# Kernel optimization log

Measured on AMD Instinct MI355X. Metric: run time of the kernel, lower is better.

## Reference

```python
import jax, jax.numpy as jnp
import numpy as np

FEATURES = 1024
DEPTH = int(np.floor(np.log2(FEATURES)))  # 10
NODES = 2 ** DEPTH - 1                    # 1023


def _unit_rows(key, shape):
    w = jax.random.normal(key, shape, dtype=jnp.float32)
    return w / jnp.linalg.norm(w, axis=-1, keepdims=True)


def setup_inputs() -> dict:
    key = jax.random.key(0)
    k_x, k_X, k_Y = jax.random.split(key, 3)
    oldx = jax.random.normal(k_x, (8, 4096, FEATURES), dtype=jnp.float32)
    X = _unit_rows(k_X, (NODES, FEATURES))  # hyperspherical-shell init
    Y = _unit_rows(k_Y, (NODES, FEATURES))
    return {"oldx": oldx, "X": X, "Y": Y}


def reference(oldx, X, Y):
    features = X.shape[-1]
    x = oldx.reshape(-1, features)            # [B, F]
    B = x.shape[0]
    cur = jnp.zeros((B,), dtype=jnp.int32)    # per-sample tree node
    y = jnp.zeros_like(x)
    for _ in range(DEPTH):                    # fixed small depth loop (10)
        Xc = X[cur]                           # [B, F] data-dependent gather
        lam = jnp.einsum('bi,bi->b', x, Xc)   # [B]
        y = y + lam[:, None] * Y[cur]         # [B, F]
        cur = cur * 2 + 1 + (lam > 0).astype(jnp.int32)
    return y.reshape(oldx.shape)
```

## Files before the change

kernel.cpp:

```cpp
#include <hip/hip_runtime.h>

#define FEAT 1024
#define DEPTH 10
#define NLEAF 1024
#define NODES (NLEAF - 1)

typedef float f32x4 __attribute__((ext_vector_type(4)));

__global__ __launch_bounds__(256) void path_kernel(
    const float* __restrict__ x,
    const float* __restrict__ Xw,
    float* __restrict__ lam_out,
    int* __restrict__ leaf_out,
    int* __restrict__ counts,
    int nsamples)
{
    const int wave = threadIdx.x >> 6;
    const int lane = threadIdx.x & 63;
    const int s = blockIdx.x * 4 + wave;
    if (s >= nsamples) return;

    const float* xp = x + (size_t)s * FEAT;
    f32x4 xv[4];
#pragma unroll
    for (int k = 0; k < 4; ++k)
        xv[k] = __builtin_nontemporal_load(
            reinterpret_cast<const f32x4*>(xp + (lane + 64 * k) * 4));

    int cur = 0;
#pragma unroll
    for (int d = 0; d < DEPTH; ++d) {
        const float* Xr = Xw + (size_t)cur * FEAT;
        double p0 = 0.0, p1 = 0.0, p2 = 0.0, p3 = 0.0;
#pragma unroll
        for (int k = 0; k < 4; ++k) {
            f32x4 xc = *reinterpret_cast<const f32x4*>(Xr + (lane + 64 * k) * 4);
            p0 += (double)xv[k][0] * (double)xc[0];
            p1 += (double)xv[k][1] * (double)xc[1];
            p2 += (double)xv[k][2] * (double)xc[2];
            p3 += (double)xv[k][3] * (double)xc[3];
        }
        double p = (p0 + p1) + (p2 + p3);
#pragma unroll
        for (int off = 32; off >= 1; off >>= 1)
            p += __shfl_xor(p, off, 64);

        if (lane == 0) lam_out[(size_t)s * DEPTH + d] = (float)p;
        cur = 2 * cur + 1 + (p > 0.0 ? 1 : 0);
    }

    if (lane == 0) {
        leaf_out[s] = cur;
        atomicAdd(&counts[cur - NODES], 1);
    }
}

__global__ __launch_bounds__(1024) void scan_kernel(
    const int* __restrict__ counts, int* __restrict__ offs, int* __restrict__ cursor)
{
    __shared__ int a[NLEAF], b[NLEAF];
    const int t = threadIdx.x;
    a[t] = counts[t];
    __syncthreads();
    int* src = a; int* dst = b;
#pragma unroll
    for (int off = 1; off < NLEAF; off <<= 1) {
        dst[t] = (t >= off) ? (src[t] + src[t - off]) : src[t];
        __syncthreads();
        int* tmp = src; src = dst; dst = tmp;
    }
    const int excl = (t == 0) ? 0 : src[t - 1];
    offs[t] = excl;
    cursor[t] = excl;
}

__global__ __launch_bounds__(256) void scatter_kernel(
    const int* __restrict__ leaf, int* __restrict__ cursor,
    int* __restrict__ order, int nsamples)
{
    int i = blockIdx.x * 256 + threadIdx.x;
    if (i < nsamples) {
        const int b = leaf[i] - NODES;
        const int pos = atomicAdd(&cursor[b], 1);
        order[pos] = i;
    }
}

__global__ __launch_bounds__(256) void emit_kernel(
    const float* __restrict__ Yw,
    const float* __restrict__ lam,
    const int* __restrict__ order,
    const int* __restrict__ offs,
    const int* __restrict__ counts,
    float* __restrict__ out)
{
    __shared__ float ylds[DEPTH][FEAT];
    const int b = blockIdx.x;
    const int leafPlus = b + NLEAF;

#pragma unroll
    for (int d = 0; d < DEPTH; ++d) {
        const int node = (leafPlus >> (DEPTH - d)) - 1;
        reinterpret_cast<f32x4*>(ylds[d])[threadIdx.x] =
            reinterpret_cast<const f32x4*>(Yw + (size_t)node * FEAT)[threadIdx.x];
    }
    __syncthreads();

    const int start = offs[b];
    const int cnt = counts[b];
    const int wave = threadIdx.x >> 6;
    const int lane = threadIdx.x & 63;

    for (int i = wave; i < cnt; i += 4) {
        const int s = order[start + i];
        float lm[DEPTH];
#pragma unroll
        for (int d = 0; d < DEPTH; ++d)
            lm[d] = lam[(size_t)s * DEPTH + d];

        float* op = out + (size_t)s * FEAT;
#pragma unroll
        for (int k = 0; k < 4; ++k) {
            f32x4 o = (f32x4)(0.f);
#pragma unroll
            for (int d = 0; d < DEPTH; ++d)
                o += lm[d] * reinterpret_cast<const f32x4*>(ylds[d])[lane + 64 * k];
            __builtin_nontemporal_store(o, reinterpret_cast<f32x4*>(op + 4 * (lane + 64 * k)));
        }
    }
}

__global__ __launch_bounds__(256) void fff_fallback(
    const float* __restrict__ x, const float* __restrict__ Xw,
    const float* __restrict__ Yw, float* __restrict__ out, int nsamples)
{
    const int wave = threadIdx.x >> 6, lane = threadIdx.x & 63;
    const int s = blockIdx.x * 4 + wave;
    if (s >= nsamples) return;
    const float* xp = x + (size_t)s * FEAT;
    f32x4 xv[4], acc[4];
#pragma unroll
    for (int k = 0; k < 4; ++k) {
        xv[k] = *reinterpret_cast<const f32x4*>(xp + (lane + 64 * k) * 4);
        acc[k] = (f32x4)(0.f);
    }
    int cur = 0;
#pragma unroll
    for (int d = 0; d < DEPTH; ++d) {
        const float* Xr = Xw + (size_t)cur * FEAT;
        double p = 0.0;
#pragma unroll
        for (int k = 0; k < 4; ++k) {
            f32x4 xc = *reinterpret_cast<const f32x4*>(Xr + (lane + 64 * k) * 4);
            p += (double)xv[k][0] * (double)xc[0];
            p += (double)xv[k][1] * (double)xc[1];
            p += (double)xv[k][2] * (double)xc[2];
            p += (double)xv[k][3] * (double)xc[3];
        }
#pragma unroll
        for (int off = 32; off >= 1; off >>= 1) p += __shfl_xor(p, off, 64);
        const float lamv = (float)p;
        const float* Yr = Yw + (size_t)cur * FEAT;
#pragma unroll
        for (int k = 0; k < 4; ++k) {
            f32x4 yc = *reinterpret_cast<const f32x4*>(Yr + (lane + 64 * k) * 4);
            acc[k] += lamv * yc;
        }
        cur = 2 * cur + 1 + (p > 0.0 ? 1 : 0);
    }
    float* op = out + (size_t)s * FEAT;
#pragma unroll
    for (int k = 0; k < 4; ++k)
        *reinterpret_cast<f32x4*>(op + 4 * (lane + 64 * k)) = acc[k];
}

extern "C" void kernel_launch(void* const* d_in, const int* in_sizes, int n_in,
                              void* d_out, int out_size, void* d_ws, size_t ws_size,
                              hipStream_t stream) {
    const float* oldx = (const float*)d_in[0];
    const float* Xw   = (const float*)d_in[1];
    const float* Yw   = (const float*)d_in[2];
    float* out = (float*)d_out;

    const int ns = in_sizes[0] / FEAT;

    const size_t lamB  = (size_t)ns * DEPTH * sizeof(float);
    const size_t leafB = (size_t)ns * sizeof(int);
    const size_t cntB  = NLEAF * sizeof(int);
    const size_t need  = lamB + leafB + 3 * cntB + leafB;

    if (ws_size < need) {
        fff_fallback<<<(ns + 3) / 4, 256, 0, stream>>>(oldx, Xw, Yw, out, ns);
        return;
    }

    char* w = (char*)d_ws;
    float* lam    = (float*)w;  w += lamB;
    int*   leaf   = (int*)w;    w += leafB;
    int*   counts = (int*)w;    w += cntB;
    int*   offs   = (int*)w;    w += cntB;
    int*   cursor = (int*)w;    w += cntB;
    int*   order  = (int*)w;

    hipMemsetAsync(counts, 0, cntB, stream);
    path_kernel<<<(ns + 3) / 4, 256, 0, stream>>>(oldx, Xw, lam, leaf, counts, ns);
    scan_kernel<<<1, 1024, 0, stream>>>(counts, offs, cursor);
    scatter_kernel<<<(ns + 255) / 256, 256, 0, stream>>>(leaf, cursor, order, ns);
    emit_kernel<<<NLEAF, 256, 0, stream>>>(Yw, lam, order, offs, counts, out);
}
```

Baseline: 122.7 us.

## Stage shallow tree rows in LDS, widen blocks, shuffle-broadcast lambdas in emit

The path kernel now runs 1024-thread blocks covering 16 samples each, and copies the first 15 tree rows of X (levels 0-3) into 60KB of shared memory. The first four depth steps read from LDS and the deeper ones still read global memory. The emit kernel moves to 512 threads and 8 waves, spreads the Y-row staging over a strided loop, and loads the ten lambdas with one lane-parallel load followed by shuffles. The aim is to cut redundant global and L2 reads of hot shallow rows and scalar lambda loads. In exchange every block must first stage 60KB, and the large LDS footprint limits occupancy.

New measurement: 126.5 us. +3.1%, slower.

```diff
diff --git a/kernel.cpp b/kernel.cpp
--- a/kernel.cpp
+++ b/kernel.cpp
@@ -4,10 +4,11 @@
 #define DEPTH 10
 #define NLEAF 1024
 #define NODES (NLEAF - 1)
+#define SHALLOW_ROWS 15
 
 typedef float f32x4 __attribute__((ext_vector_type(4)));
 
-__global__ __launch_bounds__(256) void path_kernel(
+__global__ __launch_bounds__(1024) void path_kernel(
     const float* __restrict__ x,
     const float* __restrict__ Xw,
     float* __restrict__ lam_out,
@@ -15,9 +16,16 @@
     int* __restrict__ counts,
     int nsamples)
 {
-    const int wave = threadIdx.x >> 6;
-    const int lane = threadIdx.x & 63;
-    const int s = blockIdx.x * 4 + wave;
+    __shared__ float xlds[SHALLOW_ROWS * FEAT];
+
+    const int tid = threadIdx.x;
+    for (int i = tid; i < SHALLOW_ROWS * (FEAT / 4); i += 1024)
+        reinterpret_cast<f32x4*>(xlds)[i] = reinterpret_cast<const f32x4*>(Xw)[i];
+    __syncthreads();
+
+    const int wave = tid >> 6;
+    const int lane = tid & 63;
+    const int s = blockIdx.x * 16 + wave;
     if (s >= nsamples) return;
 
     const float* xp = x + (size_t)s * FEAT;
@@ -28,9 +36,10 @@
             reinterpret_cast<const f32x4*>(xp + (lane + 64 * k) * 4));
 
     int cur = 0;
-#pragma unroll
-    for (int d = 0; d < DEPTH; ++d) {
-        const float* Xr = Xw + (size_t)cur * FEAT;
+
+#pragma unroll
+    for (int d = 0; d < 4; ++d) {
+        const float* Xr = xlds + (size_t)cur * FEAT;
         double p0 = 0.0, p1 = 0.0, p2 = 0.0, p3 = 0.0;
 #pragma unroll
         for (int k = 0; k < 4; ++k) {
@@ -44,7 +53,26 @@
 #pragma unroll
         for (int off = 32; off >= 1; off >>= 1)
             p += __shfl_xor(p, off, 64);
-
+        if (lane == 0) lam_out[(size_t)s * DEPTH + d] = (float)p;
+        cur = 2 * cur + 1 + (p > 0.0 ? 1 : 0);
+    }
+
+#pragma unroll
+    for (int d = 4; d < DEPTH; ++d) {
+        const float* Xr = Xw + (size_t)cur * FEAT;
+        double p0 = 0.0, p1 = 0.0, p2 = 0.0, p3 = 0.0;
+#pragma unroll
+        for (int k = 0; k < 4; ++k) {
+            f32x4 xc = *reinterpret_cast<const f32x4*>(Xr + (lane + 64 * k) * 4);
+            p0 += (double)xv[k][0] * (double)xc[0];
+            p1 += (double)xv[k][1] * (double)xc[1];
+            p2 += (double)xv[k][2] * (double)xc[2];
+            p3 += (double)xv[k][3] * (double)xc[3];
+        }
+        double p = (p0 + p1) + (p2 + p3);
+#pragma unroll
+        for (int off = 32; off >= 1; off >>= 1)
+            p += __shfl_xor(p, off, 64);
         if (lane == 0) lam_out[(size_t)s * DEPTH + d] = (float)p;
         cur = 2 * cur + 1 + (p > 0.0 ? 1 : 0);
     }
@@ -86,7 +114,7 @@
     }
 }
 
-__global__ __launch_bounds__(256) void emit_kernel(
+__global__ __launch_bounds__(512) void emit_kernel(
     const float* __restrict__ Yw,
     const float* __restrict__ lam,
     const int* __restrict__ order,
@@ -98,11 +126,12 @@
     const int b = blockIdx.x;
     const int leafPlus = b + NLEAF;
 
-#pragma unroll
-    for (int d = 0; d < DEPTH; ++d) {
+    for (int i = threadIdx.x; i < DEPTH * (FEAT / 4); i += 512) {
+        const int d = i >> 8;
+        const int c = i & 255;
         const int node = (leafPlus >> (DEPTH - d)) - 1;
-        reinterpret_cast<f32x4*>(ylds[d])[threadIdx.x] =
-            reinterpret_cast<const f32x4*>(Yw + (size_t)node * FEAT)[threadIdx.x];
+        reinterpret_cast<f32x4*>(ylds[d])[c] =
+            reinterpret_cast<const f32x4*>(Yw + (size_t)node * FEAT)[c];
     }
     __syncthreads();
 
@@ -111,12 +140,14 @@
     const int wave = threadIdx.x >> 6;
     const int lane = threadIdx.x & 63;
 
-    for (int i = wave; i < cnt; i += 4) {
+    for (int i = wave; i < cnt; i += 8) {
         const int s = order[start + i];
+
+        float lv = (lane < DEPTH) ? lam[(size_t)s * DEPTH + lane] : 0.0f;
         float lm[DEPTH];
 #pragma unroll
         for (int d = 0; d < DEPTH; ++d)
-            lm[d] = lam[(size_t)s * DEPTH + d];
+            lm[d] = __shfl(lv, d, 64);
 
         float* op = out + (size_t)s * FEAT;
 #pragma unroll
@@ -203,8 +234,8 @@
     int*   order  = (int*)w;
 
     hipMemsetAsync(counts, 0, cntB, stream);
-    path_kernel<<<(ns + 3) / 4, 256, 0, stream>>>(oldx, Xw, lam, leaf, counts, ns);
+    path_kernel<<<(ns + 15) / 16, 1024, 0, stream>>>(oldx, Xw, lam, leaf, counts, ns);
     scan_kernel<<<1, 1024, 0, stream>>>(counts, offs, cursor);
     scatter_kernel<<<(ns + 255) / 256, 256, 0, stream>>>(leaf, cursor, order, ns);
-    emit_kernel<<<NLEAF, 256, 0, stream>>>(Yw, lam, order, offs, counts, out);
-}
+    emit_kernel<<<NLEAF, 512, 0, stream>>>(Yw, lam, order, offs, counts, out);
+}
```

## Process two samples per wave in path kernel, DPP reduction, split emit blocks

Applied to the files above, without the earlier changes.

The path kernel now has each wave handle two samples, interleaving their gathers and FP64 dot products to raise memory-level parallelism. The shuffle-based wave reduction is replaced with DPP row operations plus a readlane. The emit kernel launches two 512-thread blocks per leaf, each taking alternate sample groups, so more waves share the staged Y rows. The trade-offs are more registers per wave, duplicate Y staging per leaf across the two blocks, and no guard for sB past nsamples when the sample count is odd.

Result: slower. 125.5 us (+2.3%).

```diff
diff --git a/kernel.cpp b/kernel.cpp
--- a/kernel.cpp
+++ b/kernel.cpp
@@ -6,6 +6,29 @@
 #define NODES (NLEAF - 1)
 
 typedef float f32x4 __attribute__((ext_vector_type(4)));
+
+template <int CTRL, int RMASK>
+__device__ __forceinline__ double dpp_shift_d(double v) {
+    union { double d; int i[2]; } u, r;
+    u.d = v;
+    r.i[0] = __builtin_amdgcn_update_dpp(0, u.i[0], CTRL, RMASK, 0xF, true);
+    r.i[1] = __builtin_amdgcn_update_dpp(0, u.i[1], CTRL, RMASK, 0xF, true);
+    return r.d;
+}
+
+__device__ __forceinline__ double wave_sum_f64(double v) {
+    v += dpp_shift_d<0x111, 0xF>(v);
+    v += dpp_shift_d<0x112, 0xF>(v);
+    v += dpp_shift_d<0x114, 0xF>(v);
+    v += dpp_shift_d<0x118, 0xF>(v);
+    v += dpp_shift_d<0x142, 0xA>(v);
+    v += dpp_shift_d<0x143, 0xC>(v);
+    union { double d; int i[2]; } u, r;
+    u.d = v;
+    r.i[0] = __builtin_amdgcn_readlane(u.i[0], 63);
+    r.i[1] = __builtin_amdgcn_readlane(u.i[1], 63);
+    return r.d;
+}
 
 __global__ __launch_bounds__(256) void path_kernel(
     const float* __restrict__ x,
@@ -17,41 +40,63 @@
 {
     const int wave = threadIdx.x >> 6;
     const int lane = threadIdx.x & 63;
-    const int s = blockIdx.x * 4 + wave;
-    if (s >= nsamples) return;
-
-    const float* xp = x + (size_t)s * FEAT;
-    f32x4 xv[4];
-#pragma unroll
-    for (int k = 0; k < 4; ++k)
-        xv[k] = __builtin_nontemporal_load(
-            reinterpret_cast<const f32x4*>(xp + (lane + 64 * k) * 4));
-
-    int cur = 0;
+    const int sA = (blockIdx.x * 4 + wave) * 2;
+    const int sB = sA + 1;
+    if (sA >= nsamples) return;
+
+    const float* xpA = x + (size_t)sA * FEAT;
+    const float* xpB = x + (size_t)sB * FEAT;
+    f32x4 xvA[4], xvB[4];
+#pragma unroll
+    for (int k = 0; k < 4; ++k) {
+        xvA[k] = __builtin_nontemporal_load(
+            reinterpret_cast<const f32x4*>(xpA + (lane + 64 * k) * 4));
+        xvB[k] = __builtin_nontemporal_load(
+            reinterpret_cast<const f32x4*>(xpB + (lane + 64 * k) * 4));
+    }
+
+    int curA = 0, curB = 0;
 #pragma unroll
     for (int d = 0; d < DEPTH; ++d) {
-        const float* Xr = Xw + (size_t)cur * FEAT;
-        double p0 = 0.0, p1 = 0.0, p2 = 0.0, p3 = 0.0;
-#pragma unroll
-        for (int k = 0; k < 4; ++k) {
-            f32x4 xc = *reinterpret_cast<const f32x4*>(Xr + (lane + 64 * k) * 4);
-            p0 += (double)xv[k][0] * (double)xc[0];
-            p1 += (double)xv[k][1] * (double)xc[1];
-            p2 += (double)xv[k][2] * (double)xc[2];
-            p3 += (double)xv[k][3] * (double)xc[3];
-        }
-        double p = (p0 + p1) + (p2 + p3);
-#pragma unroll
-        for (int off = 32; off >= 1; off >>= 1)
-            p += __shfl_xor(p, off, 64);
-
-        if (lane == 0) lam_out[(size_t)s * DEPTH + d] = (float)p;
-        cur = 2 * cur + 1 + (p > 0.0 ? 1 : 0);
+        const float* XrA = Xw + (size_t)curA * FEAT;
+        const float* XrB = Xw + (size_t)curB * FEAT;
+
+        f32x4 xcA[4], xcB[4];
+#pragma unroll
+        for (int k = 0; k < 4; ++k) {
+            xcA[k] = *reinterpret_cast<const f32x4*>(XrA + (lane + 64 * k) * 4);
+            xcB[k] = *reinterpret_cast<const f32x4*>(XrB + (lane + 64 * k) * 4);
+        }
+
+        double a0 = 0.0, a1 = 0.0, a2 = 0.0, a3 = 0.0;
+        double b0 = 0.0, b1 = 0.0, b2 = 0.0, b3 = 0.0;
+#pragma unroll
+        for (int k = 0; k < 4; ++k) {
+            a0 += (double)xvA[k][0] * (double)xcA[k][0];
+            a1 += (double)xvA[k][1] * (double)xcA[k][1];
+            a2 += (double)xvA[k][2] * (double)xcA[k][2];
+            a3 += (double)xvA[k][3] * (double)xcA[k][3];
+            b0 += (double)xvB[k][0] * (double)xcB[k][0];
+            b1 += (double)xvB[k][1] * (double)xcB[k][1];
+            b2 += (double)xvB[k][2] * (double)xcB[k][2];
+            b3 += (double)xvB[k][3] * (double)xcB[k][3];
+        }
+        double pA = wave_sum_f64((a0 + a1) + (a2 + a3));
+        double pB = wave_sum_f64((b0 + b1) + (b2 + b3));
+
+        if (lane == 0) {
+            lam_out[(size_t)sA * DEPTH + d] = (float)pA;
+            lam_out[(size_t)sB * DEPTH + d] = (float)pB;
+        }
+        curA = 2 * curA + 1 + (pA > 0.0 ? 1 : 0);
+        curB = 2 * curB + 1 + (pB > 0.0 ? 1 : 0);
     }
 
     if (lane == 0) {
-        leaf_out[s] = cur;
-        atomicAdd(&counts[cur - NODES], 1);
+        leaf_out[sA] = curA;
+        leaf_out[sB] = curB;
+        atomicAdd(&counts[curA - NODES], 1);
+        atomicAdd(&counts[curB - NODES], 1);
     }
 }
 
@@ -86,7 +131,7 @@
     }
 }
 
-__global__ __launch_bounds__(256) void emit_kernel(
+__global__ __launch_bounds__(512) void emit_kernel(
     const float* __restrict__ Yw,
     const float* __restrict__ lam,
     const int* __restrict__ order,
@@ -95,14 +140,16 @@
     float* __restrict__ out)
 {
     __shared__ float ylds[DEPTH][FEAT];
-    const int b = blockIdx.x;
+    const int b = blockIdx.x >> 1;
+    const int half = blockIdx.x & 1;
     const int leafPlus = b + NLEAF;
 
-#pragma unroll
-    for (int d = 0; d < DEPTH; ++d) {
+    for (int i = threadIdx.x; i < DEPTH * (FEAT / 4); i += 512) {
+        const int d = i >> 8;
+        const int c = i & 255;
         const int node = (leafPlus >> (DEPTH - d)) - 1;
-        reinterpret_cast<f32x4*>(ylds[d])[threadIdx.x] =
-            reinterpret_cast<const f32x4*>(Yw + (size_t)node * FEAT)[threadIdx.x];
+        reinterpret_cast<f32x4*>(ylds[d])[c] =
+            reinterpret_cast<const f32x4*>(Yw + (size_t)node * FEAT)[c];
     }
     __syncthreads();
 
@@ -111,12 +158,14 @@
     const int wave = threadIdx.x >> 6;
     const int lane = threadIdx.x & 63;
 
-    for (int i = wave; i < cnt; i += 4) {
-        const int s = order[start + i];
+    for (int i = half * 8 + wave; i < cnt; i += 16) {
+        const int s = __builtin_amdgcn_readfirstlane(order[start + i]);
+
+        const float* lp = lam + (size_t)s * DEPTH;
         float lm[DEPTH];
 #pragma unroll
         for (int d = 0; d < DEPTH; ++d)
-            lm[d] = lam[(size_t)s * DEPTH + d];
+            lm[d] = lp[d];
 
         float* op = out + (size_t)s * FEAT;
 #pragma unroll
@@ -202,9 +251,9 @@
     int*   cursor = (int*)w;    w += cntB;
     int*   order  = (int*)w;
 
-    hipMemsetAsync(counts, 0, cntB, stream);
-    path_kernel<<<(ns + 3) / 4, 256, 0, stream>>>(oldx, Xw, lam, leaf, counts, ns);
+    (void)hipMemsetAsync(counts, 0, cntB, stream);
+    path_kernel<<<(ns + 7) / 8, 256, 0, stream>>>(oldx, Xw, lam, leaf, counts, ns);
     scan_kernel<<<1, 1024, 0, stream>>>(counts, offs, cursor);
     scatter_kernel<<<(ns + 255) / 256, 256, 0, stream>>>(leaf, cursor, order, ns);
-    emit_kernel<<<NLEAF, 256, 0, stream>>>(Yw, lam, order, offs, counts, out);
-}
+    emit_kernel<<<2 * NLEAF, 512, 0, stream>>>(Yw, lam, order, offs, counts, out);
+}
```
